# Performance work log

Measured on AMD Instinct MI355X. Metric: run time of the kernel, lower is better.

Reference implementation:

```python
import jax, jax.numpy as jnp
import numpy as np

EMB = 128
HEAD = 8
QKV = 16
SQRT_EMB = 11.313708498984761
CLIP = 10.0
B, P, N = 64, 100, 1000


def setup_inputs() -> dict:
    key = jax.random.key(0)
    ks = jax.random.split(key, 12)
    encoded_last_node = jax.random.normal(ks[0], (B, P, EMB), jnp.float32)
    load = jax.random.uniform(ks[1], (B, P), jnp.float32)
    time = jax.random.uniform(ks[2], (B, P), jnp.float32)
    cur_dist = jax.random.uniform(ks[3], (B, P, N), jnp.float32)
    mask_bits = jax.random.uniform(ks[4], (B, P, N)) < 0.1
    ninf_mask = jnp.where(mask_bits, -1e9, 0.0).astype(jnp.float32)
    noise = jax.random.uniform(ks[5], (B, P, N), jnp.float32)
    encoded_nodes = jax.random.normal(ks[6], (B, N, EMB), jnp.float32)
    s = 1.0 / np.sqrt(EMB)
    Wq = jax.random.uniform(ks[7], (EMB + 2, HEAD * QKV), jnp.float32, -s, s)
    Wk = jax.random.uniform(ks[8], (EMB, HEAD * QKV), jnp.float32, -s, s)
    Wv = jax.random.uniform(ks[9], (EMB, HEAD * QKV), jnp.float32, -s, s)
    Wc = jax.random.uniform(ks[10], (HEAD * QKV, EMB), jnp.float32, -s, s)
    bc = jax.random.uniform(ks[11], (EMB,), jnp.float32, -s, s)
    return {"encoded_last_node": encoded_last_node, "load": load, "time": time,
            "cur_dist": cur_dist, "ninf_mask": ninf_mask, "noise": noise,
            "encoded_nodes": encoded_nodes, "Wq": Wq, "Wk": Wk, "Wv": Wv,
            "Wc": Wc, "bc": bc}


def _heads(x):
    # (B, n, H*D) -> (B, H, n, D)
    b, n, _ = x.shape
    return x.reshape(b, n, HEAD, QKV).transpose(0, 2, 1, 3)


def reference(encoded_last_node, load, time, cur_dist, ninf_mask, noise,
              encoded_nodes, Wq, Wk, Wv, Wc, bc):
    # set_kv
    k = _heads(encoded_nodes @ Wk)   # (B,H,N,D)
    v = _heads(encoded_nodes @ Wv)   # (B,H,N,D)

    # query from last node + load + time
    input_cat = jnp.concatenate(
        [encoded_last_node, load[:, :, None], time[:, :, None]], axis=2)
    q = _heads(input_cat @ Wq)       # (B,H,P,D)

    # multi-head attention with rank3 ninf mask
    score = jnp.einsum('bhpd,bhnd->bhpn', q, k) / jnp.sqrt(
        jnp.asarray(QKV, jnp.float32))
    score = score + ninf_mask[:, None, :, :]
    weights = jax.nn.softmax(score, axis=3)
    out = jnp.einsum('bhpn,bhnd->bhpd', weights, v)
    out_concat = out.transpose(0, 2, 1, 3).reshape(B, P, HEAD * QKV)
    mh_atten_out = out_concat @ Wc + bc            # (B,P,EMB)

    # single-head pointer logits
    score2 = jnp.einsum('bpe,bne->bpn', mh_atten_out, encoded_nodes)
    score_scaled = score2 / SQRT_EMB

    # heuristic / noise blend
    st_cost = cur_dist + cur_dist
    raw_heuristic = -jnp.log(st_cost + 1e-6)
    a = 1.0 / (1.0 + 2.0 ** ((100.0 - N) / 50.0))
    b = 1.0 - a
    mixed_signal = a * raw_heuristic + b * noise
    s = score_scaled + mixed_signal
    score_clipped = CLIP * jnp.tanh(s)
    score_masked = score_clipped + ninf_mask
    probs = jax.nn.softmax(score_masked, axis=2)
    return probs
```

## Files before the change

### kernel.cpp

```cpp
#include <hip/hip_runtime.h>
#include <hip/hip_bf16.h>

#define B_   64
#define P_   100
#define N_   1000
#define EMB_ 128
#define HEAD_ 8
#define QKV_ 16
#define QT   4

constexpr double kTwoPowNeg18 = 3.814697265625e-06;
constexpr double kA_d = 1.0 / (1.0 + kTwoPowNeg18);

__global__ __launch_bounds__(256) void kv_proj(
    const float* __restrict__ en, const float* __restrict__ Wk,
    const float* __restrict__ Wv, float* __restrict__ K2, float* __restrict__ V2)
{
    __shared__ __align__(16) float e_s[32][128];
    const int t = threadIdx.x;
    const int j = t & 127;
    const int half = t >> 7;
    const int r0 = blockIdx.x * 32;

    {
        const float4* src = (const float4*)(en + (size_t)r0 * 128);
        float4* dst = (float4*)&e_s[0][0];
        #pragma unroll
        for (int k = 0; k < 4; ++k) dst[t + 256 * k] = src[t + 256 * k];
    }
    __syncthreads();

    float ak[16], av[16];
    #pragma unroll
    for (int r = 0; r < 16; ++r) { ak[r] = 0.f; av[r] = 0.f; }

    const int rb = half * 16;
    for (int i4 = 0; i4 < 32; ++i4) {
        float wk4[4], wv4[4];
        #pragma unroll
        for (int c = 0; c < 4; ++c) {
            wk4[c] = Wk[(4 * i4 + c) * 128 + j];
            wv4[c] = Wv[(4 * i4 + c) * 128 + j];
        }
        #pragma unroll
        for (int r = 0; r < 16; ++r) {
            const float4 e4 = *(const float4*)&e_s[rb + r][4 * i4];
            ak[r] = fmaf(e4.x, wk4[0], fmaf(e4.y, wk4[1],
                    fmaf(e4.z, wk4[2], fmaf(e4.w, wk4[3], ak[r]))));
            av[r] = fmaf(e4.x, wv4[0], fmaf(e4.y, wv4[1],
                    fmaf(e4.z, wv4[2], fmaf(e4.w, wv4[3], av[r]))));
        }
    }

    const int h = j >> 4, d = j & 15;
    #pragma unroll
    for (int r = 0; r < 16; ++r) {
        const int row = r0 + rb + r;
        const int bb = row / N_;
        const int n = row - bb * N_;
        const size_t idx = ((size_t)(bb * HEAD_ + h) * N_ + n) * 16 + d;
        K2[idx] = ak[r];
        V2[idx] = av[r];
    }
}

__global__ __launch_bounds__(128) void q_proj(
    const float* __restrict__ eln, const float* __restrict__ load_,
    const float* __restrict__ time_, const float* __restrict__ Wq,
    float* __restrict__ Q)
{
    __shared__ __align__(16) float e_s[8][132];
    const int j  = threadIdx.x;
    const int r0 = blockIdx.x * 8;

    #pragma unroll
    for (int r = 0; r < 8; ++r) {
        const int row = r0 + r;
        e_s[r][j] = eln[(size_t)row * 128 + j];
        if (j == 0) {
            e_s[r][128] = load_[row];
            e_s[r][129] = time_[row];
        }
    }
    __syncthreads();

    float a[8];
    #pragma unroll
    for (int r = 0; r < 8; ++r) a[r] = 0.f;

    for (int i4 = 0; i4 < 32; ++i4) {
        float w4[4];
        #pragma unroll
        for (int c = 0; c < 4; ++c) w4[c] = Wq[(4 * i4 + c) * 128 + j];
        #pragma unroll
        for (int r = 0; r < 8; ++r) {
            const float4 e4 = *(const float4*)&e_s[r][4 * i4];
            a[r] = fmaf(e4.x, w4[0], fmaf(e4.y, w4[1],
                   fmaf(e4.z, w4[2], fmaf(e4.w, w4[3], a[r]))));
        }
    }
    #pragma unroll
    for (int i = 128; i < 130; ++i) {
        const float w = Wq[i * 128 + j];
        #pragma unroll
        for (int r = 0; r < 8; ++r)
            a[r] = fmaf(e_s[r][i], w, a[r]);
    }

    #pragma unroll
    for (int r = 0; r < 8; ++r)
        Q[(size_t)(r0 + r) * 128 + j] = a[r];
}

__global__ __launch_bounds__(256) void attn_heads(
    const float* __restrict__ K2, const float* __restrict__ V2,
    const float* __restrict__ Q, const float* __restrict__ ninf,
    float* __restrict__ out_g)
{
    __shared__ __align__(16) float sc[QT][1008];
    __shared__ __align__(16) float q_s[QT][16];
    __shared__ __align__(16) float part_s[4][QT][16];
    __shared__ float invden_s[QT];

    const int blk = blockIdx.x;
    const int b   = blk / (HEAD_ * 25);
    const int rem = blk - b * (HEAD_ * 25);
    const int h   = rem / 25;
    const int pt  = rem - h * 25;
    const int bp0 = b * P_ + pt * QT;
    const int t    = threadIdx.x;
    const int lane = t & 63;
    const int wv   = t >> 6;

    if (t < 64) q_s[t >> 4][t & 15] =
        Q[(size_t)(bp0 + (t >> 4)) * 128 + h * 16 + (t & 15)];
    __syncthreads();

    float qr[QT][16];
    #pragma unroll
    for (int q = 0; q < QT; ++q)
        #pragma unroll
        for (int c = 0; c < 4; ++c)
            *(float4*)&qr[q][4 * c] = *(const float4*)&q_s[q][4 * c];

    const float* nf0 = ninf + (size_t)bp0 * N_;
    float msk[QT][4];
    #pragma unroll
    for (int i = 0; i < 4; ++i) {
        const int n = t + 256 * i;
        if (n < N_) {
            #pragma unroll
            for (int q = 0; q < QT; ++q) msk[q][i] = nf0[q * N_ + n];
        }
    }

    const float* Kh = K2 + (size_t)(b * HEAD_ + h) * N_ * 16;
    #pragma unroll
    for (int i = 0; i < 4; ++i) {
        const int n = t + 256 * i;
        if (n < N_) {
            const float4* kr = (const float4*)(Kh + (size_t)n * 16);
            const float4 k0 = kr[0], k1 = kr[1], k2 = kr[2], k3 = kr[3];
            #pragma unroll
            for (int q = 0; q < QT; ++q) {
                float d = k0.x * qr[q][0]  + k0.y * qr[q][1]
                        + k0.z * qr[q][2]  + k0.w * qr[q][3]
                        + k1.x * qr[q][4]  + k1.y * qr[q][5]
                        + k1.z * qr[q][6]  + k1.w * qr[q][7]
                        + k2.x * qr[q][8]  + k2.y * qr[q][9]
                        + k2.z * qr[q][10] + k2.w * qr[q][11]
                        + k3.x * qr[q][12] + k3.y * qr[q][13]
                        + k3.z * qr[q][14] + k3.w * qr[q][15];
                sc[q][n] = d * 0.25f + msk[q][i];
            }
        }
    }
    __syncthreads();

    {
        const int q = wv;
        float m = -INFINITY;
        for (int n = lane; n < N_; n += 64) m = fmaxf(m, sc[q][n]);
        #pragma unroll
        for (int off = 32; off > 0; off >>= 1) m = fmaxf(m, __shfl_xor(m, off));
        float s = 0.f;
        for (int n = lane; n < N_; n += 64) {
            const float e = __expf(sc[q][n] - m);
            sc[q][n] = e;
            s += e;
        }
        #pragma unroll
        for (int off = 32; off > 0; off >>= 1) s += __shfl_xor(s, off);
        if (lane == 0) invden_s[q] = 1.f / s;
    }
    __syncthreads();

    {
        const int c = lane & 3, g = lane >> 2;
        const float* Vh = V2 + (size_t)(b * HEAD_ + h) * N_ * 16 + 4 * c;
        const int n0 = wv * 250;
        float4 a0 = {0.f, 0.f, 0.f, 0.f}, a1 = a0, a2 = a0, a3 = a0;
        #pragma unroll 4
        for (int i = 0; i < 16; ++i) {
            const int nn = 16 * i + g;
            if (nn < 250) {
                const int n = n0 + nn;
                const float4 v4 = *(const float4*)(Vh + (size_t)n * 16);
                const float w0 = sc[0][n], w1 = sc[1][n];
                const float w2 = sc[2][n], w3 = sc[3][n];
                a0.x = fmaf(w0, v4.x, a0.x); a0.y = fmaf(w0, v4.y, a0.y);
                a0.z = fmaf(w0, v4.z, a0.z); a0.w = fmaf(w0, v4.w, a0.w);
                a1.x = fmaf(w1, v4.x, a1.x); a1.y = fmaf(w1, v4.y, a1.y);
                a1.z = fmaf(w1, v4.z, a1.z); a1.w = fmaf(w1, v4.w, a1.w);
                a2.x = fmaf(w2, v4.x, a2.x); a2.y = fmaf(w2, v4.y, a2.y);
                a2.z = fmaf(w2, v4.z, a2.z); a2.w = fmaf(w2, v4.w, a2.w);
                a3.x = fmaf(w3, v4.x, a3.x); a3.y = fmaf(w3, v4.y, a3.y);
                a3.z = fmaf(w3, v4.z, a3.z); a3.w = fmaf(w3, v4.w, a3.w);
            }
        }
        #pragma unroll
        for (int off = 4; off <= 32; off <<= 1) {
            a0.x += __shfl_xor(a0.x, off); a0.y += __shfl_xor(a0.y, off);
            a0.z += __shfl_xor(a0.z, off); a0.w += __shfl_xor(a0.w, off);
            a1.x += __shfl_xor(a1.x, off); a1.y += __shfl_xor(a1.y, off);
            a1.z += __shfl_xor(a1.z, off); a1.w += __shfl_xor(a1.w, off);
            a2.x += __shfl_xor(a2.x, off); a2.y += __shfl_xor(a2.y, off);
            a2.z += __shfl_xor(a2.z, off); a2.w += __shfl_xor(a2.w, off);
            a3.x += __shfl_xor(a3.x, off); a3.y += __shfl_xor(a3.y, off);
            a3.z += __shfl_xor(a3.z, off); a3.w += __shfl_xor(a3.w, off);
        }
        if (g == 0) {
            *(float4*)&part_s[wv][0][4 * c] = a0;
            *(float4*)&part_s[wv][1][4 * c] = a1;
            *(float4*)&part_s[wv][2][4 * c] = a2;
            *(float4*)&part_s[wv][3][4 * c] = a3;
        }
    }
    __syncthreads();

    if (t < 64) {
        const int q = t >> 4, d = t & 15;
        const float s = part_s[0][q][d] + part_s[1][q][d]
                      + part_s[2][q][d] + part_s[3][q][d];
        out_g[(size_t)(bp0 + q) * 128 + h * 16 + d] = s * invden_s[q];
    }
}

__global__ __launch_bounds__(256) void ptr_epilogue(
    const float* __restrict__ out_g, const float* __restrict__ en,
    const float* __restrict__ Wc, const float* __restrict__ bc,
    const float* __restrict__ cur_dist, const float* __restrict__ ninf,
    const float* __restrict__ noise, float* __restrict__ probs)
{
    __shared__ __align__(16) float sc[QT][1008];
    __shared__ __align__(16) float out_s[QT][128];
    __shared__ __align__(16) float mh_s[QT][128];

    const int blk  = blockIdx.x;
    const int b    = blk / 25;
    const int pt   = blk - b * 25;
    const int bp0  = b * P_ + pt * QT;
    const int t    = threadIdx.x;
    const int lane = t & 63;
    const int wv   = t >> 6;

    if (t < 128)
        ((float4*)&out_s[0][0])[t] = ((const float4*)(out_g + (size_t)bp0 * 128))[t];
    __syncthreads();

    {
        const int e = t & 127, qh = t >> 7;
        float a0 = bc[e], a1 = a0;
        for (int i = 0; i < 128; ++i) {
            const float w = Wc[i * 128 + e];
            a0 = fmaf(out_s[qh][i], w, a0);
            a1 = fmaf(out_s[qh + 2][i], w, a1);
        }
        mh_s[qh][e] = a0;
        mh_s[qh + 2][e] = a1;
    }
    __syncthreads();

    const float* Eb = en + (size_t)b * N_ * 128;
    const float4* m0 = (const float4*)mh_s[0];
    const float4* m1 = (const float4*)mh_s[1];
    const float4* m2 = (const float4*)mh_s[2];
    const float4* m3 = (const float4*)mh_s[3];
    #pragma unroll
    for (int half = 0; half < 2; ++half) {
        const int na = t + half * 512;
        const int nb = na + 256;
        const bool vb = (nb < N_);
        const float4* ea = (const float4*)(Eb + (size_t)na * 128);
        const float4* eb = (const float4*)(Eb + (size_t)(vb ? nb : na) * 128);
        float d0a = 0.f, d1a = 0.f, d2a = 0.f, d3a = 0.f;
        float d0b = 0.f, d1b = 0.f, d2b = 0.f, d3b = 0.f;
        #pragma unroll 4
        for (int i = 0; i < 32; ++i) {
            const float4 A4 = m0[i], B4 = m1[i], C4 = m2[i], D4 = m3[i];
            const float4 e1 = ea[i];
            const float4 e2 = eb[i];
            d0a += e1.x * A4.x + e1.y * A4.y + e1.z * A4.z + e1.w * A4.w;
            d1a += e1.x * B4.x + e1.y * B4.y + e1.z * B4.z + e1.w * B4.w;
            d2a += e1.x * C4.x + e1.y * C4.y + e1.z * C4.z + e1.w * C4.w;
            d3a += e1.x * D4.x + e1.y * D4.y + e1.z * D4.z + e1.w * D4.w;
            d0b += e2.x * A4.x + e2.y * A4.y + e2.z * A4.z + e2.w * A4.w;
            d1b += e2.x * B4.x + e2.y * B4.y + e2.z * B4.z + e2.w * B4.w;
            d2b += e2.x * C4.x + e2.y * C4.y + e2.z * C4.z + e2.w * C4.w;
            d3b += e2.x * D4.x + e2.y * D4.y + e2.z * D4.z + e2.w * D4.w;
        }
        sc[0][na] = d0a; sc[1][na] = d1a; sc[2][na] = d2a; sc[3][na] = d3a;
        if (vb) { sc[0][nb] = d0b; sc[1][nb] = d1b; sc[2][nb] = d2b; sc[3][nb] = d3b; }
    }
    __syncthreads();

    {
        const int q  = wv;
        const int bp = bp0 + q;
        const float* cd = cur_dist + (size_t)bp * N_;
        const float* nz = noise    + (size_t)bp * N_;
        const float* nf = ninf     + (size_t)bp * N_;
        const float A   = (float)kA_d;
        const float Bc2 = (float)(1.0 - kA_d);

        float m = -INFINITY;
        for (int n = lane; n < N_; n += 64) {
            const float s2 = sc[q][n] / 11.3137085f;
            const float st = cd[n] + cd[n];
            const float rh = -logf(st + 1e-6f);
            const float s  = s2 + A * rh + Bc2 * nz[n];
            const float sm = 10.f * tanhf(s) + nf[n];
            sc[q][n] = sm;
            m = fmaxf(m, sm);
        }
        #pragma unroll
        for (int off = 32; off > 0; off >>= 1) m = fmaxf(m, __shfl_xor(m, off));

        float s = 0.f;
        for (int n = lane; n < N_; n += 64) {
            const float e = __expf(sc[q][n] - m);
            sc[q][n] = e;
            s += e;
        }
        #pragma unroll
        for (int off = 32; off > 0; off >>= 1) s += __shfl_xor(s, off);

        const float inv = 1.f / s;
        float* out = probs + (size_t)bp * N_;
        for (int n = lane; n < N_; n += 64) out[n] = sc[q][n] * inv;
    }
}

extern "C" void kernel_launch(void* const* d_in, const int* in_sizes, int n_in,
                              void* d_out, int out_size, void* d_ws, size_t ws_size,
                              hipStream_t stream)
{
    const float* eln      = (const float*)d_in[0];
    const float* load_    = (const float*)d_in[1];
    const float* time_    = (const float*)d_in[2];
    const float* cur_dist = (const float*)d_in[3];
    const float* ninf     = (const float*)d_in[4];
    const float* noise    = (const float*)d_in[5];
    const float* en       = (const float*)d_in[6];
    const float* Wq       = (const float*)d_in[7];
    const float* Wk       = (const float*)d_in[8];
    const float* Wv       = (const float*)d_in[9];
    const float* Wc       = (const float*)d_in[10];
    const float* bc       = (const float*)d_in[11];
    float* probs = (float*)d_out;

    float* K2    = (float*)d_ws;
    float* V2    = K2 + (size_t)B_ * HEAD_ * N_ * 16;
    float* Q     = V2 + (size_t)B_ * HEAD_ * N_ * 16;
    float* out_g = Q  + (size_t)B_ * P_ * 128;

    kv_proj<<<(B_ * N_) / 32, 256, 0, stream>>>(en, Wk, Wv, K2, V2);
    q_proj<<<(B_ * P_) / 8, 128, 0, stream>>>(eln, load_, time_, Wq, Q);
    attn_heads<<<B_ * HEAD_ * (P_ / QT), 256, 0, stream>>>(K2, V2, Q, ninf, out_g);
    ptr_epilogue<<<(B_ * P_) / QT, 256, 0, stream>>>(out_g, en, Wc, bc,
                                                     cur_dist, ninf, noise, probs);
}
```

Before: 549.5 us.

## Stage encoded_nodes tiles through LDS with prefetch and remap block order

The pointer-score stage in ptr_epilogue now streams encoded_nodes through a padded shared-memory tile of 32 rows, register-prefetching the next tile while computing. Eight threads cooperate on each row, and a shuffle reduction replaces the old per-thread strided float4 row reads, which coalesced poorly. Block index mapping in both attn_heads and ptr_epilogue is reordered so neighbouring blocks share cache-resident K/V or batch data differently. This adds synchronisation per tile and extra LDS usage, which may reduce occupancy.

```diff
diff --git a/kernel.cpp b/kernel.cpp
--- a/kernel.cpp
+++ b/kernel.cpp
@@ -123,10 +123,10 @@
     __shared__ float invden_s[QT];
 
     const int blk = blockIdx.x;
-    const int b   = blk / (HEAD_ * 25);
-    const int rem = blk - b * (HEAD_ * 25);
-    const int h   = rem / 25;
-    const int pt  = rem - h * 25;
+    const int h   = blk & 7;
+    const int j9  = blk >> 3;
+    const int pt  = j9 % 25;
+    const int b   = j9 / 25;
     const int bp0 = b * P_ + pt * QT;
     const int t    = threadIdx.x;
     const int lane = t & 63;
@@ -252,13 +252,16 @@
     const float* __restrict__ cur_dist, const float* __restrict__ ninf,
     const float* __restrict__ noise, float* __restrict__ probs)
 {
+    __shared__ __align__(16) float en_s[32 * 132];
     __shared__ __align__(16) float sc[QT][1008];
     __shared__ __align__(16) float out_s[QT][128];
     __shared__ __align__(16) float mh_s[QT][128];
 
     const int blk  = blockIdx.x;
-    const int b    = blk / 25;
-    const int pt   = blk - b * 25;
+    const int rX   = blk & 7;
+    const int j9   = blk >> 3;
+    const int pt   = j9 % 25;
+    const int b    = (j9 / 25) * 8 + rX;
     const int bp0  = b * P_ + pt * QT;
     const int t    = threadIdx.x;
     const int lane = t & 63;
@@ -281,36 +284,62 @@
     }
     __syncthreads();
 
-    const float* Eb = en + (size_t)b * N_ * 128;
-    const float4* m0 = (const float4*)mh_s[0];
-    const float4* m1 = (const float4*)mh_s[1];
-    const float4* m2 = (const float4*)mh_s[2];
-    const float4* m3 = (const float4*)mh_s[3];
-    #pragma unroll
-    for (int half = 0; half < 2; ++half) {
-        const int na = t + half * 512;
-        const int nb = na + 256;
-        const bool vb = (nb < N_);
-        const float4* ea = (const float4*)(Eb + (size_t)na * 128);
-        const float4* eb = (const float4*)(Eb + (size_t)(vb ? nb : na) * 128);
-        float d0a = 0.f, d1a = 0.f, d2a = 0.f, d3a = 0.f;
-        float d0b = 0.f, d1b = 0.f, d2b = 0.f, d3b = 0.f;
-        #pragma unroll 4
-        for (int i = 0; i < 32; ++i) {
-            const float4 A4 = m0[i], B4 = m1[i], C4 = m2[i], D4 = m3[i];
-            const float4 e1 = ea[i];
-            const float4 e2 = eb[i];
-            d0a += e1.x * A4.x + e1.y * A4.y + e1.z * A4.z + e1.w * A4.w;
-            d1a += e1.x * B4.x + e1.y * B4.y + e1.z * B4.z + e1.w * B4.w;
-            d2a += e1.x * C4.x + e1.y * C4.y + e1.z * C4.z + e1.w * C4.w;
-            d3a += e1.x * D4.x + e1.y * D4.y + e1.z * D4.z + e1.w * D4.w;
-            d0b += e2.x * A4.x + e2.y * A4.y + e2.z * A4.z + e2.w * A4.w;
-            d1b += e2.x * B4.x + e2.y * B4.y + e2.z * B4.z + e2.w * B4.w;
-            d2b += e2.x * C4.x + e2.y * C4.y + e2.z * C4.z + e2.w * C4.w;
-            d3b += e2.x * D4.x + e2.y * D4.y + e2.z * D4.z + e2.w * D4.w;
-        }
-        sc[0][na] = d0a; sc[1][na] = d1a; sc[2][na] = d2a; sc[3][na] = d3a;
-        if (vb) { sc[0][nb] = d0b; sc[1][nb] = d1b; sc[2][nb] = d2b; sc[3][nb] = d3b; }
+    const int row = t >> 3, c = t & 7;
+    float4 mhr[QT][4];
+    #pragma unroll
+    for (int q = 0; q < QT; ++q)
+        #pragma unroll
+        for (int jj = 0; jj < 4; ++jj)
+            mhr[q][jj] = *(const float4*)&mh_s[q][c * 16 + 4 * jj];
+
+    const float* enb = en + (size_t)b * N_ * 128;
+    float4 pre[4];
+    {
+        const float4* g = (const float4*)enb;
+        #pragma unroll
+        for (int k = 0; k < 4; ++k) pre[k] = g[t + 256 * k];
+    }
+    for (int n0 = 0; n0 < N_; n0 += 32) {
+        const int rows = (N_ - n0 < 32) ? (N_ - n0) : 32;
+        __syncthreads();
+        #pragma unroll
+        for (int k = 0; k < 4; ++k) {
+            const int L = t + 256 * k;
+            if (L < rows * 32)
+                *(float4*)&en_s[(L >> 5) * 132 + (L & 31) * 4] = pre[k];
+        }
+        const int n1 = n0 + 32;
+        if (n1 < N_) {
+            const int rows1 = (N_ - n1 < 32) ? (N_ - n1) : 32;
+            const float4* g = (const float4*)(enb + (size_t)n1 * 128);
+            #pragma unroll
+            for (int k = 0; k < 4; ++k) {
+                const int L = t + 256 * k;
+                if (L < rows1 * 32) pre[k] = g[L];
+            }
+        }
+        __syncthreads();
+        if (row < rows) {
+            float acc[QT] = {0.f, 0.f, 0.f, 0.f};
+            #pragma unroll
+            for (int jj = 0; jj < 4; ++jj) {
+                const float4 e4 = *(const float4*)&en_s[row * 132 + c * 16 + 4 * jj];
+                #pragma unroll
+                for (int q = 0; q < QT; ++q) {
+                    acc[q] = fmaf(e4.x, mhr[q][jj].x, fmaf(e4.y, mhr[q][jj].y,
+                             fmaf(e4.z, mhr[q][jj].z, fmaf(e4.w, mhr[q][jj].w,
+                             acc[q]))));
+                }
+            }
+            #pragma unroll
+            for (int q = 0; q < QT; ++q) {
+                float v = acc[q];
+                v += __shfl_xor(v, 1);
+                v += __shfl_xor(v, 2);
+                v += __shfl_xor(v, 4);
+                if (c == 0) sc[q][n0 + row] = v;
+            }
+        }
     }
     __syncthreads();
 
```

After: 673.0 us. +22.5%, slower.
